# Kernel tuning notes

Measured on AMD Instinct MI355X. Metric: run time of the kernel, lower is better.

## Reference

```python
import jax, jax.numpy as jnp
import numpy as np

Q = 9          # D2Q9
G = 8          # dihedral group of the square
X = YD = 768   # spatial grid
HID = 32       # tau_net hidden width
N_IN = 6       # moments with order <= 2 (indices 0..5, contiguous by construction)
LOWER_TAU = 0.8


def _build_stencil():
    # D2Q9 velocities and weights
    e = np.array([[0, 0], [1, 0], [0, 1], [-1, 0], [0, -1],
                  [1, 1], [-1, 1], [-1, -1], [1, -1]], dtype=np.float64)
    w = np.array([4 / 9] + [1 / 9] * 4 + [1 / 36] * 4, dtype=np.float64)
    # natural moment matrix: rows are monomials ex^px * ey^py, ordered so that
    # moment_order = [0,1,1,2,2,2,3,3,4]  ->  in_indices=[0..5], out_indices=[6,7,8]
    exps = [(0, 0), (1, 0), (0, 1), (2, 0), (1, 1), (0, 2), (2, 1), (1, 2), (2, 2)]
    M = np.stack([e[:, 0] ** px * e[:, 1] ** py for px, py in exps])  # [Q, Q]
    Minv = np.linalg.inv(M)
    # symmetry group of the square: 4 rotations x {id, x-axis reflection}
    rots = [np.array([[np.cos(a), -np.sin(a)], [np.sin(a), np.cos(a)]])
            for a in (0.0, np.pi / 2, np.pi, 3 * np.pi / 2)]
    refl = np.array([[1.0, 0.0], [0.0, -1.0]])
    Rs = rots + [r @ refl for r in rots]
    perms = []
    for R in Rs:
        Re = np.rint(e @ R.T)
        P = np.zeros((Q, Q))
        for i in range(Q):
            j = int(np.where((e == Re[i]).all(axis=1))[0][0])
            P[j, i] = 1.0  # velocity i maps to velocity j under R
        perms.append(P)
    P = np.stack(perms)                                   # [G, Q, Q]
    actions = np.einsum('qp,gpr,rs->gqs', M, P, Minv)      # moment action  M P M^-1
    Pt = P.transpose(0, 2, 1)                              # P^-1 = P^T
    inv_actions = np.einsum('qp,gpr,rs->gqs', M, Pt, Minv)
    return (M.astype(np.float32), Minv.astype(np.float32),
            actions.astype(np.float32), inv_actions.astype(np.float32),
            e.astype(np.float32), w.astype(np.float32))


def setup_inputs() -> dict:
    key = jax.random.key(0)
    kf, k1, k2, k3 = jax.random.split(key, 4)
    M, Minv, actions, inv_actions, e, w = _build_stencil()
    f = jax.random.uniform(kf, (Q, X, YD), dtype=jnp.float32)
    s = 0.1
    return {
        'f': f,
        'M': jnp.asarray(M), 'Minv': jnp.asarray(Minv),
        'actions': jnp.asarray(actions), 'inv_actions': jnp.asarray(inv_actions),
        'e': jnp.asarray(e), 'w': jnp.asarray(w),
        'W1': jax.random.normal(k1, (N_IN, HID), jnp.float32) * s,
        'b1': jnp.zeros((HID,), jnp.float32),
        'W2': jax.random.normal(k2, (HID, HID), jnp.float32) * s,
        'b2': jnp.zeros((HID,), jnp.float32),
        'W3': jax.random.normal(k3, (HID, Q - N_IN), jnp.float32) * s,
        'b3': jnp.zeros((Q - N_IN,), jnp.float32),
    }


def reference(f, M, Minv, actions, inv_actions, e, w, W1, b1, W2, b2, W3, b3):
    # --- moment transform: m = M f, moved to channel-last [X, Y, Q] ---
    m = jnp.einsum('qp,pxy->xyq', M, f)
    # --- equivariant tau net on low-order moments ---
    x_in = m[..., :N_IN]                                   # in_indices = 0..5
    Ainv = inv_actions[:, :N_IN, :N_IN]                    # [G, 6, 6]
    A = actions[:, N_IN:, N_IN:]                           # [G, 3, 3] (out_indices)
    xg = jnp.einsum('gij,xyj->gxyi', Ainv, x_in)           # [G, X, Y, 6]
    h = jax.nn.relu(xg @ W1 + b1)
    h = jax.nn.relu(h @ W2 + b2)
    o = h @ W3 + b3                                        # [G, X, Y, 3]
    out = jnp.einsum('gij,gxyj->xyi', A, o)                # sum over group -> [X, Y, 3]
    tau_hi = 1.5 + jax.nn.elu(out)                         # gt_half: > 0.5
    taus = jnp.full(m.shape, LOWER_TAU, m.dtype).at[..., N_IN:].set(tau_hi)
    # --- equilibrium moments: meq = M feq(rho, u) (quadratic BGK, cs^2=1/3) ---
    rho = m[..., 0:1]                                      # natural moments: m0=rho
    u = m[..., 1:3] / rho                                  # m1,m2 = momentum
    eu = jnp.einsum('qd,xyd->xyq', e, u)
    usq = jnp.sum(u * u, axis=-1, keepdims=True)
    feq = w * rho * (1.0 + 3.0 * eu + 4.5 * eu * eu - 1.5 * usq)
    meq = jnp.einsum('qp,xyp->xyq', M, feq)
    # --- MRT collision + inverse transform ---
    m_post = m - (m - meq) / taus
    return jnp.einsum('pq,xyq->pxy', Minv, m_post)
```

## Files before the change

kernel.cpp:

```cpp
#include <hip/hip_runtime.h>
#include <hip/hip_bf16.h>
#include <math.h>

#define Q 9
#define NPIX (768 * 768)

typedef short bf16x8 __attribute__((ext_vector_type(8)));
typedef short s16x2 __attribute__((ext_vector_type(2)));
typedef float f32x4 __attribute__((ext_vector_type(4)));
typedef float f32x16 __attribute__((ext_vector_type(16)));
typedef int i32x4 __attribute__((ext_vector_type(4)));

#define A3LOV 512
#define A3HIV 1024
#define A2LOV 1536
#define A2HIV 1600
#define B3TF  6656
#define WSHORTS 13312
#define WVEC4   (WSHORTS / 8)

__device__ __forceinline__ int hidmap(int k) {
    return (k & 3) + 8 * ((k >> 2) & 1) + 4 * (k >> 3);
}

__device__ __forceinline__ unsigned short f2bf(float x) {
    unsigned u = __builtin_bit_cast(unsigned, x);
    unsigned r = u + 0x7FFFu + ((u >> 16) & 1u);
    return (unsigned short)(r >> 16);
}

__device__ __forceinline__ unsigned pk2(float e, float o) {
    __hip_bfloat162 h = __float22bfloat162_rn(make_float2(e, o));
    unsigned u;
    __builtin_memcpy(&u, &h, 4);
    return u;
}

__device__ __forceinline__ unsigned relu2(unsigned d) {
    s16x2 v = __builtin_bit_cast(s16x2, d);
    const s16x2 z = {0, 0};
    v = __builtin_elementwise_max(v, z);
    return __builtin_bit_cast(unsigned, v);
}

__device__ __forceinline__ bf16x8 mk8(unsigned w0, unsigned w1, unsigned w2, unsigned w3) {
    i32x4 t = {(int)w0, (int)w1, (int)w2, (int)w3};
    return __builtin_bit_cast(bf16x8, t);
}

__global__ void prep_kernel(const float* __restrict__ actions,
                            const float* __restrict__ inv_actions,
                            const float* __restrict__ W1,
                            const float* __restrict__ b1,
                            const float* __restrict__ W2,
                            const float* __restrict__ W3,
                            const float* __restrict__ b3,
                            short* __restrict__ wsb,
                            float* __restrict__ wsf) {
    const int idx = blockIdx.x * 256 + threadIdx.x;
    if (idx < 4096) {
        int j = idx & 7, l = (idx >> 3) & 63, g = idx >> 9;
        int m = l & 31, k = (l >> 5) * 8 + j;
        float v = 0.f;
        if (k < 6) {
            #pragma unroll
            for (int i = 0; i < 6; i++)
                v += inv_actions[g * 81 + i * 9 + k] * W1[i * 32 + m];
        } else if (k == 6) v = b1[m];
        wsb[idx] = (short)f2bf(v);
    } else if (idx < 8192) {
        int t = idx - 4096;
        int j = t & 7, l = (t >> 3) & 63, g = t >> 9;
        int m = l & 31, kk = (l >> 5) * 8 + j, h = hidmap(kk);
        float v = 0.f;
        if (m < 3) {
            #pragma unroll
            for (int j3 = 0; j3 < 3; j3++)
                v += W3[h * 3 + j3] * actions[g * 81 + (6 + m) * 9 + (6 + j3)];
        }
        wsb[idx] = (short)f2bf(v);
    } else if (idx < 12288) {
        int t = idx - 8192;
        int j = t & 7, l = (t >> 3) & 63, g = t >> 9;
        int m = l & 31, kk = (l >> 5) * 8 + j, h = 16 + hidmap(kk);
        float v = 0.f;
        if (m < 3) {
            #pragma unroll
            for (int j3 = 0; j3 < 3; j3++)
                v += W3[h * 3 + j3] * actions[g * 81 + (6 + m) * 9 + (6 + j3)];
        }
        wsb[idx] = (short)f2bf(v);
    } else if (idx < 12800) {
        int t = idx - 12288;
        int j = t & 7, l = (t >> 3) & 63;
        int m = l & 31, kk = (l >> 5) * 8 + j;
        wsb[idx] = (short)f2bf(W2[hidmap(kk) * 32 + m]);
    } else if (idx < 13312) {
        int t = idx - 12800;
        int j = t & 7, l = (t >> 3) & 63;
        int m = l & 31, kk = (l >> 5) * 8 + j;
        wsb[idx] = (short)f2bf(W2[(16 + hidmap(kk)) * 32 + m]);
    } else if (idx < 13315) {
        int t = idx - 13312;
        float acc = 0.f;
        for (int g = 0; g < 8; g++)
            #pragma unroll
            for (int j = 0; j < 3; j++)
                acc += actions[g * 81 + (6 + t) * 9 + (6 + j)] * b3[j];
        wsf[B3TF + t] = acc;
    }
}

#define MLP_BODY(WA1, W3LO, W3HI, B1F, OACC)                                          \
    {                                                                                 \
        f32x16 C1 = __builtin_amdgcn_mfma_f32_32x32x16_bf16(WA1, B1F, z16, 0, 0, 0);  \
        bf16x8 B2lo = mk8(relu2(pk2(C1[0], C1[1])), relu2(pk2(C1[2], C1[3])),         \
                          relu2(pk2(C1[4], C1[5])), relu2(pk2(C1[6], C1[7])));        \
        bf16x8 B2hi = mk8(relu2(pk2(C1[8], C1[9])), relu2(pk2(C1[10], C1[11])),       \
                          relu2(pk2(C1[12], C1[13])), relu2(pk2(C1[14], C1[15])));    \
        f32x16 C2 = __builtin_amdgcn_mfma_f32_32x32x16_bf16(a2hi, B2hi, c2i, 0, 0, 0);\
        C2 = __builtin_amdgcn_mfma_f32_32x32x16_bf16(a2lo, B2lo, C2, 0, 0, 0);        \
        bf16x8 B3lo = mk8(relu2(pk2(C2[0], C2[1])), relu2(pk2(C2[2], C2[3])),         \
                          relu2(pk2(C2[4], C2[5])), relu2(pk2(C2[6], C2[7])));        \
        bf16x8 B3hi = mk8(relu2(pk2(C2[8], C2[9])), relu2(pk2(C2[10], C2[11])),       \
                          relu2(pk2(C2[12], C2[13])), relu2(pk2(C2[14], C2[15])));    \
        OACC = __builtin_amdgcn_mfma_f32_32x32x16_bf16(W3HI, B3hi, OACC, 0, 0, 0);    \
        OACC = __builtin_amdgcn_mfma_f32_32x32x16_bf16(W3LO, B3lo, OACC, 0, 0, 0);    \
    }

__global__ __launch_bounds__(256, 3) void lbm_kernel(
    const float* __restrict__ f,
    const float* __restrict__ Minv,
    const float* __restrict__ w,
    const float* __restrict__ b2,
    const short* __restrict__ wsb,
    const float* __restrict__ wsf,
    float* __restrict__ out) {
    __shared__ float oL[4][64][4];
    __shared__ __align__(16) short wlds[WSHORTS];
    (void)Minv;
    (void)w;

    const int tid = threadIdx.x;
    const int wv = tid >> 6;
    const int l = tid & 63;
    const int hi = l >> 5;
    const int p = blockIdx.x * 256 + tid;

    {
        const i32x4* src = (const i32x4*)wsb;
        i32x4* dst = (i32x4*)wlds;
        #pragma unroll
        for (int i = tid; i < WVEC4; i += 256) dst[i] = src[i];
    }

    float fv0 = f[0 * NPIX + p], fv1 = f[1 * NPIX + p], fv2 = f[2 * NPIX + p];
    float fv3 = f[3 * NPIX + p], fv4 = f[4 * NPIX + p], fv5 = f[5 * NPIX + p];
    float fv6 = f[6 * NPIX + p], fv7 = f[7 * NPIX + p], fv8 = f[8 * NPIX + p];
    float sa = fv5 + fv6, sb = fv7 + fv8, sc = fv5 - fv6, sd = fv7 - fv8;
    float sab = sa + sb;
    float m4 = sc + sd;
    float p13 = fv1 + fv3, d13 = fv1 - fv3, p24 = fv2 + fv4, d24 = fv2 - fv4;
    float m0 = fv0 + p13 + p24 + sab;
    float m1 = d13 + (sc - sd);
    float m2 = d24 + (sa - sb);
    float m3 = p13 + sab;
    float m5 = p24 + sab;

    unsigned mp0 = pk2(m0, m1), mp1 = pk2(m2, m3), mp2 = pk2(m4, m5);
    const unsigned CONE = 0x00003F80u;
    const int s0 = (l & 31) << 2;
    const int s1 = s0 | (32 << 2);
    bf16x8 B1A = mk8((unsigned)__builtin_amdgcn_ds_bpermute(s0, (int)mp0),
                     (unsigned)__builtin_amdgcn_ds_bpermute(s0, (int)mp1),
                     (unsigned)__builtin_amdgcn_ds_bpermute(s0, (int)mp2), CONE);
    bf16x8 B1B = mk8((unsigned)__builtin_amdgcn_ds_bpermute(s1, (int)mp0),
                     (unsigned)__builtin_amdgcn_ds_bpermute(s1, (int)mp1),
                     (unsigned)__builtin_amdgcn_ds_bpermute(s1, (int)mp2), CONE);

    float b30 = wsf[B3TF + 0], b31 = wsf[B3TF + 1], b32 = wsf[B3TF + 2];
    f32x16 c2i;
    #pragma unroll
    for (int r = 0; r < 16; r++) {
        const int base = (r & 3) + 8 * (r >> 2);
        c2i[r] = hi ? b2[base + 4] : b2[base];
    }
    f32x16 oinit;
    #pragma unroll
    for (int r = 0; r < 16; r++) oinit[r] = 0.f;
    oinit[0] = hi ? 0.f : b30;
    oinit[1] = hi ? 0.f : b31;
    oinit[2] = hi ? 0.f : b32;
    f32x16 oaccA = oinit, oaccB = oinit;
    f32x16 z16;
    #pragma unroll
    for (int r = 0; r < 16; r++) z16[r] = 0.f;

    __syncthreads();
    const bf16x8* wl = (const bf16x8*)wlds;
    bf16x8 a2lo = wl[A2LOV + l], a2hi = wl[A2HIV + l];

    bf16x8 wa1 = wl[l], w3lo = wl[A3LOV + l], w3hi = wl[A3HIV + l];
    #pragma unroll 1
    for (int g = 0; g < 7; g++) {
        const int gn = g + 1;
        bf16x8 na1  = wl[gn * 64 + l];
        bf16x8 n3lo = wl[A3LOV + gn * 64 + l];
        bf16x8 n3hi = wl[A3HIV + gn * 64 + l];
        MLP_BODY(wa1, w3lo, w3hi, B1A, oaccA);
        MLP_BODY(wa1, w3lo, w3hi, B1B, oaccB);
        wa1 = na1; w3lo = n3lo; w3hi = n3hi;
    }
    int p2 = p;
    asm("" : "+v"(p2));
    float fr0 = f[0 * NPIX + p2], fr1 = f[1 * NPIX + p2], fr2 = f[2 * NPIX + p2];
    float fr3 = f[3 * NPIX + p2], fr4 = f[4 * NPIX + p2], fr5 = f[5 * NPIX + p2];
    float fr6 = f[6 * NPIX + p2], fr7 = f[7 * NPIX + p2], fr8 = f[8 * NPIX + p2];
    MLP_BODY(wa1, w3lo, w3hi, B1A, oaccA);
    MLP_BODY(wa1, w3lo, w3hi, B1B, oaccB);

    if (hi == 0) {
        f32x4 t0 = {oaccA[0], oaccA[1], oaccA[2], oaccA[3]};
        *(f32x4*)&oL[wv][l & 31][0] = t0;
        f32x4 t1 = {oaccB[0], oaccB[1], oaccB[2], oaccB[3]};
        *(f32x4*)&oL[wv][32 + (l & 31)][0] = t1;
    }
    f32x4 ov = *(const f32x4*)&oL[wv][l][0];

    float tinv[3];
    #pragma unroll
    for (int i = 0; i < 3; i++) {
        float o = ov[i];
        float el = (o > 0.f) ? o : (__expf(o) - 1.f);
        tinv[i] = __builtin_amdgcn_rcpf(1.5f + el);
    }

    float rho = m0;
    float ir = __builtin_amdgcn_rcpf(rho);
    float ux = m1 * ir, uy = m2 * ir;
    float usq = ux * ux + uy * uy;
    float base = 1.f - 1.5f * usq;
    float w1r = rho * (1.f / 9.f), w5r = rho * (1.f / 36.f);
    float bx = 3.f * ux, ax = fmaf(4.5f * ux, ux, base);
    float feq1 = w1r * (ax + bx), feq3 = w1r * (ax - bx);
    float by = 3.f * uy, ay = fmaf(4.5f * uy, uy, base);
    float feq2 = w1r * (ay + by), feq4 = w1r * (ay - by);
    float ss = ux + uy, bs = 3.f * ss, as_ = fmaf(4.5f * ss, ss, base);
    float feq5 = w5r * (as_ + bs), feq7 = w5r * (as_ - bs);
    float dd = uy - ux, bd = 3.f * dd, ad = fmaf(4.5f * dd, dd, base);
    float feq6 = w5r * (ad + bd), feq8 = w5r * (ad - bd);

    float g1 = fr1 - feq1, g2 = fr2 - feq2, g3 = fr3 - feq3, g4 = fr4 - feq4;
    float g5 = fr5 - feq5, g6 = fr6 - feq6, g7 = fr7 - feq7, g8 = fr8 - feq8;
    float pa = g1 + g3, pb = g2 + g4;
    float ea = g5 + g6, eb = g7 + g8, ec = g5 - g6, ed = g7 - g8;
    float eab = ea + eb;
    float m3p = pa + eab, m5p = pb + eab, m8p = eab;
    float m6p = ea - eb, m4p = ec + ed, m7p = ec - ed;

    float d3 = 1.25f * m3p, h3 = 0.625f * m3p;
    float d5 = 1.25f * m5p, h5 = 0.625f * m5p;
    float k4 = 0.3125f * m4p;
    float h6 = (0.5f * tinv[0]) * m6p, k6 = 0.5f * h6;
    float h7 = (0.5f * tinv[1]) * m7p, k7 = 0.5f * h7;
    float d8 = tinv[2] * m8p, h8 = 0.5f * d8, k8 = 0.5f * h8;

    float c0 = d8 - d3 - d5;
    float c1 = h3 - h7 - h8;
    float c2 = h5 - h6 - h8;
    float c3 = h3 + h7 - h8;
    float c4 = h5 + h6 - h8;
    float sA = k4 + k7, sB = k6 + k8, sC = k4 + k8;
    float sD = k6 + k7, sE = k7 + k8, sF = k4 + k6;
    float c5 = sA + sB, c6 = sB - sA, c7 = sC - sD, c8 = sE - sF;

    __builtin_nontemporal_store(fr0 - c0, &out[0 * NPIX + p]);
    __builtin_nontemporal_store(fr1 - c1, &out[1 * NPIX + p]);
    __builtin_nontemporal_store(fr2 - c2, &out[2 * NPIX + p]);
    __builtin_nontemporal_store(fr3 - c3, &out[3 * NPIX + p]);
    __builtin_nontemporal_store(fr4 - c4, &out[4 * NPIX + p]);
    __builtin_nontemporal_store(fr5 - c5, &out[5 * NPIX + p]);
    __builtin_nontemporal_store(fr6 - c6, &out[6 * NPIX + p]);
    __builtin_nontemporal_store(fr7 - c7, &out[7 * NPIX + p]);
    __builtin_nontemporal_store(fr8 - c8, &out[8 * NPIX + p]);
}

extern "C" void kernel_launch(void* const* d_in, const int* in_sizes, int n_in,
                              void* d_out, int out_size, void* d_ws, size_t ws_size,
                              hipStream_t stream) {
    const float* f           = (const float*)d_in[0];
    const float* Minv        = (const float*)d_in[2];
    const float* actions     = (const float*)d_in[3];
    const float* inv_actions = (const float*)d_in[4];
    const float* w           = (const float*)d_in[6];
    const float* W1          = (const float*)d_in[7];
    const float* b1          = (const float*)d_in[8];
    const float* W2          = (const float*)d_in[9];
    const float* b2          = (const float*)d_in[10];
    const float* W3          = (const float*)d_in[11];
    const float* b3          = (const float*)d_in[12];
    float* outp = (float*)d_out;
    short* wsb = (short*)d_ws;
    float* wsf = (float*)d_ws;

    prep_kernel<<<53, 256, 0, stream>>>(actions, inv_actions, W1, b1, W2, W3, b3, wsb, wsf);
    lbm_kernel<<<NPIX / 256, 256, 0, stream>>>(f, Minv, w, b2, wsb, wsf, outp);
}
```

Baseline: 119.6 us.

## Process two pixel tiles per block to amortize weight staging across more MLP work

Each 256-thread block now handles 512 pixels. Each wave runs four interleaved MLP chains per group iteration instead of two, reusing the LDS-loaded weight fragments, and the grid is halved. This amortizes the per-block weight copy into LDS and the per-iteration weight loads, and gives more independent MFMA work to hide latency. The epilogue re-derives rho and velocity from the reloaded f, so fewer values stay live across the loop. The cost is higher register pressure from four accumulators under a 3-blocks-per-CU launch bound, with possible spills or lower occupancy, plus fewer blocks in flight.

```diff
diff --git a/kernel.cpp b/kernel.cpp
--- a/kernel.cpp
+++ b/kernel.cpp
@@ -128,105 +128,24 @@
         OACC = __builtin_amdgcn_mfma_f32_32x32x16_bf16(W3LO, B3lo, OACC, 0, 0, 0);    \
     }
 
-__global__ __launch_bounds__(256, 3) void lbm_kernel(
-    const float* __restrict__ f,
-    const float* __restrict__ Minv,
-    const float* __restrict__ w,
-    const float* __restrict__ b2,
-    const short* __restrict__ wsb,
-    const float* __restrict__ wsf,
-    float* __restrict__ out) {
-    __shared__ float oL[4][64][4];
-    __shared__ __align__(16) short wlds[WSHORTS];
-    (void)Minv;
-    (void)w;
-
-    const int tid = threadIdx.x;
-    const int wv = tid >> 6;
-    const int l = tid & 63;
-    const int hi = l >> 5;
-    const int p = blockIdx.x * 256 + tid;
-
-    {
-        const i32x4* src = (const i32x4*)wsb;
-        i32x4* dst = (i32x4*)wlds;
-        #pragma unroll
-        for (int i = tid; i < WVEC4; i += 256) dst[i] = src[i];
-    }
-
-    float fv0 = f[0 * NPIX + p], fv1 = f[1 * NPIX + p], fv2 = f[2 * NPIX + p];
-    float fv3 = f[3 * NPIX + p], fv4 = f[4 * NPIX + p], fv5 = f[5 * NPIX + p];
-    float fv6 = f[6 * NPIX + p], fv7 = f[7 * NPIX + p], fv8 = f[8 * NPIX + p];
-    float sa = fv5 + fv6, sb = fv7 + fv8, sc = fv5 - fv6, sd = fv7 - fv8;
-    float sab = sa + sb;
-    float m4 = sc + sd;
-    float p13 = fv1 + fv3, d13 = fv1 - fv3, p24 = fv2 + fv4, d24 = fv2 - fv4;
-    float m0 = fv0 + p13 + p24 + sab;
-    float m1 = d13 + (sc - sd);
-    float m2 = d24 + (sa - sb);
-    float m3 = p13 + sab;
-    float m5 = p24 + sab;
-
-    unsigned mp0 = pk2(m0, m1), mp1 = pk2(m2, m3), mp2 = pk2(m4, m5);
-    const unsigned CONE = 0x00003F80u;
-    const int s0 = (l & 31) << 2;
-    const int s1 = s0 | (32 << 2);
-    bf16x8 B1A = mk8((unsigned)__builtin_amdgcn_ds_bpermute(s0, (int)mp0),
-                     (unsigned)__builtin_amdgcn_ds_bpermute(s0, (int)mp1),
-                     (unsigned)__builtin_amdgcn_ds_bpermute(s0, (int)mp2), CONE);
-    bf16x8 B1B = mk8((unsigned)__builtin_amdgcn_ds_bpermute(s1, (int)mp0),
-                     (unsigned)__builtin_amdgcn_ds_bpermute(s1, (int)mp1),
-                     (unsigned)__builtin_amdgcn_ds_bpermute(s1, (int)mp2), CONE);
-
-    float b30 = wsf[B3TF + 0], b31 = wsf[B3TF + 1], b32 = wsf[B3TF + 2];
-    f32x16 c2i;
-    #pragma unroll
-    for (int r = 0; r < 16; r++) {
-        const int base = (r & 3) + 8 * (r >> 2);
-        c2i[r] = hi ? b2[base + 4] : b2[base];
-    }
-    f32x16 oinit;
-    #pragma unroll
-    for (int r = 0; r < 16; r++) oinit[r] = 0.f;
-    oinit[0] = hi ? 0.f : b30;
-    oinit[1] = hi ? 0.f : b31;
-    oinit[2] = hi ? 0.f : b32;
-    f32x16 oaccA = oinit, oaccB = oinit;
-    f32x16 z16;
-    #pragma unroll
-    for (int r = 0; r < 16; r++) z16[r] = 0.f;
-
-    __syncthreads();
-    const bf16x8* wl = (const bf16x8*)wlds;
-    bf16x8 a2lo = wl[A2LOV + l], a2hi = wl[A2HIV + l];
-
-    bf16x8 wa1 = wl[l], w3lo = wl[A3LOV + l], w3hi = wl[A3HIV + l];
-    #pragma unroll 1
-    for (int g = 0; g < 7; g++) {
-        const int gn = g + 1;
-        bf16x8 na1  = wl[gn * 64 + l];
-        bf16x8 n3lo = wl[A3LOV + gn * 64 + l];
-        bf16x8 n3hi = wl[A3HIV + gn * 64 + l];
-        MLP_BODY(wa1, w3lo, w3hi, B1A, oaccA);
-        MLP_BODY(wa1, w3lo, w3hi, B1B, oaccB);
-        wa1 = na1; w3lo = n3lo; w3hi = n3hi;
-    }
-    int p2 = p;
-    asm("" : "+v"(p2));
-    float fr0 = f[0 * NPIX + p2], fr1 = f[1 * NPIX + p2], fr2 = f[2 * NPIX + p2];
-    float fr3 = f[3 * NPIX + p2], fr4 = f[4 * NPIX + p2], fr5 = f[5 * NPIX + p2];
-    float fr6 = f[6 * NPIX + p2], fr7 = f[7 * NPIX + p2], fr8 = f[8 * NPIX + p2];
-    MLP_BODY(wa1, w3lo, w3hi, B1A, oaccA);
-    MLP_BODY(wa1, w3lo, w3hi, B1B, oaccB);
-
-    if (hi == 0) {
-        f32x4 t0 = {oaccA[0], oaccA[1], oaccA[2], oaccA[3]};
-        *(f32x4*)&oL[wv][l & 31][0] = t0;
-        f32x4 t1 = {oaccB[0], oaccB[1], oaccB[2], oaccB[3]};
-        *(f32x4*)&oL[wv][32 + (l & 31)][0] = t1;
-    }
-    f32x4 ov = *(const f32x4*)&oL[wv][l][0];
-
+#define MOMENTS_PK(F0,F1,F2,F3,F4,F5,F6,F7,F8, MP0, MP1, MP2)                         \
+    {                                                                                 \
+        float sa = F5 + F6, sb = F7 + F8, sc = F5 - F6, sd = F7 - F8;                 \
+        float sab = sa + sb;                                                          \
+        float m4_ = sc + sd;                                                          \
+        float p13 = F1 + F3, d13 = F1 - F3, p24 = F2 + F4, d24 = F2 - F4;             \
+        float m0_ = F0 + p13 + p24 + sab;                                             \
+        float m1_ = d13 + (sc - sd);                                                  \
+        float m2_ = d24 + (sa - sb);                                                  \
+        float m3_ = p13 + sab;                                                        \
+        float m5_ = p24 + sab;                                                        \
+        MP0 = pk2(m0_, m1_); MP1 = pk2(m2_, m3_); MP2 = pk2(m4_, m5_);                \
+    }
+
+__device__ __forceinline__ void epilogue(float fr0, float fr1, float fr2, float fr3,
+                                         float fr4, float fr5, float fr6, float fr7,
+                                         float fr8, f32x4 ov, int p,
+                                         float* __restrict__ out) {
     float tinv[3];
     #pragma unroll
     for (int i = 0; i < 3; i++) {
@@ -234,8 +153,12 @@
         float el = (o > 0.f) ? o : (__expf(o) - 1.f);
         tinv[i] = __builtin_amdgcn_rcpf(1.5f + el);
     }
-
-    float rho = m0;
+    float sa = fr5 + fr6, sb = fr7 + fr8, sc = fr5 - fr6, sd = fr7 - fr8;
+    float p13 = fr1 + fr3, p24 = fr2 + fr4;
+    float rho = fr0 + p13 + p24 + (sa + sb);
+    float m1 = (fr1 - fr3) + (sc - sd);
+    float m2 = (fr2 - fr4) + (sa - sb);
+
     float ir = __builtin_amdgcn_rcpf(rho);
     float ux = m1 * ir, uy = m2 * ir;
     float usq = ux * ux + uy * uy;
@@ -283,6 +206,127 @@
     __builtin_nontemporal_store(fr6 - c6, &out[6 * NPIX + p]);
     __builtin_nontemporal_store(fr7 - c7, &out[7 * NPIX + p]);
     __builtin_nontemporal_store(fr8 - c8, &out[8 * NPIX + p]);
+}
+
+__global__ __launch_bounds__(256, 3) void lbm_kernel(
+    const float* __restrict__ f,
+    const float* __restrict__ Minv,
+    const float* __restrict__ w,
+    const float* __restrict__ b2,
+    const short* __restrict__ wsb,
+    const float* __restrict__ wsf,
+    float* __restrict__ out) {
+    __shared__ float oL[4][128][4];
+    __shared__ __align__(16) short wlds[WSHORTS];
+    (void)Minv;
+    (void)w;
+
+    const int tid = threadIdx.x;
+    const int wv = tid >> 6;
+    const int l = tid & 63;
+    const int hi = l >> 5;
+    const int p0 = blockIdx.x * 512 + tid;
+    const int p1 = p0 + 256;
+
+    {
+        const i32x4* src = (const i32x4*)wsb;
+        i32x4* dst = (i32x4*)wlds;
+        for (int i = tid; i < WVEC4; i += 256) dst[i] = src[i];
+    }
+
+    unsigned mp0a, mp1a, mp2a, mp0b, mp1b, mp2b;
+    {
+        float a0 = f[0 * NPIX + p0], a1 = f[1 * NPIX + p0], a2 = f[2 * NPIX + p0];
+        float a3 = f[3 * NPIX + p0], a4 = f[4 * NPIX + p0], a5 = f[5 * NPIX + p0];
+        float a6 = f[6 * NPIX + p0], a7 = f[7 * NPIX + p0], a8 = f[8 * NPIX + p0];
+        MOMENTS_PK(a0, a1, a2, a3, a4, a5, a6, a7, a8, mp0a, mp1a, mp2a);
+        float b0 = f[0 * NPIX + p1], b1v = f[1 * NPIX + p1], b2v = f[2 * NPIX + p1];
+        float b3v = f[3 * NPIX + p1], b4 = f[4 * NPIX + p1], b5 = f[5 * NPIX + p1];
+        float b6 = f[6 * NPIX + p1], b7 = f[7 * NPIX + p1], b8 = f[8 * NPIX + p1];
+        MOMENTS_PK(b0, b1v, b2v, b3v, b4, b5, b6, b7, b8, mp0b, mp1b, mp2b);
+    }
+
+    const unsigned CONE = 0x00003F80u;
+    const int s0 = (l & 31) << 2;
+    const int s1 = s0 | (32 << 2);
+    bf16x8 B1A0 = mk8((unsigned)__builtin_amdgcn_ds_bpermute(s0, (int)mp0a),
+                      (unsigned)__builtin_amdgcn_ds_bpermute(s0, (int)mp1a),
+                      (unsigned)__builtin_amdgcn_ds_bpermute(s0, (int)mp2a), CONE);
+    bf16x8 B1B0 = mk8((unsigned)__builtin_amdgcn_ds_bpermute(s1, (int)mp0a),
+                      (unsigned)__builtin_amdgcn_ds_bpermute(s1, (int)mp1a),
+                      (unsigned)__builtin_amdgcn_ds_bpermute(s1, (int)mp2a), CONE);
+    bf16x8 B1A1 = mk8((unsigned)__builtin_amdgcn_ds_bpermute(s0, (int)mp0b),
+                      (unsigned)__builtin_amdgcn_ds_bpermute(s0, (int)mp1b),
+                      (unsigned)__builtin_amdgcn_ds_bpermute(s0, (int)mp2b), CONE);
+    bf16x8 B1B1 = mk8((unsigned)__builtin_amdgcn_ds_bpermute(s1, (int)mp0b),
+                      (unsigned)__builtin_amdgcn_ds_bpermute(s1, (int)mp1b),
+                      (unsigned)__builtin_amdgcn_ds_bpermute(s1, (int)mp2b), CONE);
+
+    float b30 = wsf[B3TF + 0], b31 = wsf[B3TF + 1], b32 = wsf[B3TF + 2];
+    f32x16 c2i;
+    #pragma unroll
+    for (int r = 0; r < 16; r++) {
+        const int base = (r & 3) + 8 * (r >> 2);
+        c2i[r] = hi ? b2[base + 4] : b2[base];
+    }
+    f32x16 oinit;
+    #pragma unroll
+    for (int r = 0; r < 16; r++) oinit[r] = 0.f;
+    oinit[0] = hi ? 0.f : b30;
+    oinit[1] = hi ? 0.f : b31;
+    oinit[2] = hi ? 0.f : b32;
+    f32x16 oaccA0 = oinit, oaccB0 = oinit, oaccA1 = oinit, oaccB1 = oinit;
+    f32x16 z16;
+    #pragma unroll
+    for (int r = 0; r < 16; r++) z16[r] = 0.f;
+
+    __syncthreads();
+    const bf16x8* wl = (const bf16x8*)wlds;
+    bf16x8 a2lo = wl[A2LOV + l], a2hi = wl[A2HIV + l];
+
+    bf16x8 wa1 = wl[l], w3lo = wl[A3LOV + l], w3hi = wl[A3HIV + l];
+    #pragma unroll 1
+    for (int g = 0; g < 7; g++) {
+        const int gn = g + 1;
+        bf16x8 na1  = wl[gn * 64 + l];
+        bf16x8 n3lo = wl[A3LOV + gn * 64 + l];
+        bf16x8 n3hi = wl[A3HIV + gn * 64 + l];
+        MLP_BODY(wa1, w3lo, w3hi, B1A0, oaccA0);
+        MLP_BODY(wa1, w3lo, w3hi, B1B0, oaccB0);
+        MLP_BODY(wa1, w3lo, w3hi, B1A1, oaccA1);
+        MLP_BODY(wa1, w3lo, w3hi, B1B1, oaccB1);
+        wa1 = na1; w3lo = n3lo; w3hi = n3hi;
+    }
+    int q0 = p0;
+    asm("" : "+v"(q0));
+    const int q1 = q0 + 256;
+    float r00 = f[0 * NPIX + q0], r01 = f[1 * NPIX + q0], r02 = f[2 * NPIX + q0];
+    float r03 = f[3 * NPIX + q0], r04 = f[4 * NPIX + q0], r05 = f[5 * NPIX + q0];
+    float r06 = f[6 * NPIX + q0], r07 = f[7 * NPIX + q0], r08 = f[8 * NPIX + q0];
+    float r10 = f[0 * NPIX + q1], r11 = f[1 * NPIX + q1], r12 = f[2 * NPIX + q1];
+    float r13 = f[3 * NPIX + q1], r14 = f[4 * NPIX + q1], r15 = f[5 * NPIX + q1];
+    float r16 = f[6 * NPIX + q1], r17 = f[7 * NPIX + q1], r18 = f[8 * NPIX + q1];
+    MLP_BODY(wa1, w3lo, w3hi, B1A0, oaccA0);
+    MLP_BODY(wa1, w3lo, w3hi, B1B0, oaccB0);
+    MLP_BODY(wa1, w3lo, w3hi, B1A1, oaccA1);
+    MLP_BODY(wa1, w3lo, w3hi, B1B1, oaccB1);
+
+    if (hi == 0) {
+        const int lc = l & 31;
+        f32x4 t0 = {oaccA0[0], oaccA0[1], oaccA0[2], oaccA0[3]};
+        *(f32x4*)&oL[wv][lc][0] = t0;
+        f32x4 t1 = {oaccB0[0], oaccB0[1], oaccB0[2], oaccB0[3]};
+        *(f32x4*)&oL[wv][32 + lc][0] = t1;
+        f32x4 t2 = {oaccA1[0], oaccA1[1], oaccA1[2], oaccA1[3]};
+        *(f32x4*)&oL[wv][64 + lc][0] = t2;
+        f32x4 t3 = {oaccB1[0], oaccB1[1], oaccB1[2], oaccB1[3]};
+        *(f32x4*)&oL[wv][96 + lc][0] = t3;
+    }
+    f32x4 ov0 = *(const f32x4*)&oL[wv][l][0];
+    f32x4 ov1 = *(const f32x4*)&oL[wv][64 + l][0];
+
+    epilogue(r00, r01, r02, r03, r04, r05, r06, r07, r08, ov0, p0, out);
+    epilogue(r10, r11, r12, r13, r14, r15, r16, r17, r18, ov1, p1, out);
 }
 
 extern "C" void kernel_launch(void* const* d_in, const int* in_sizes, int n_in,
@@ -304,5 +348,5 @@
     float* wsf = (float*)d_ws;
 
     prep_kernel<<<53, 256, 0, stream>>>(actions, inv_actions, W1, b1, W2, W3, b3, wsb, wsf);
-    lbm_kernel<<<NPIX / 256, 256, 0, stream>>>(f, Minv, w, b2, wsb, wsf, outp);
-}
+    lbm_kernel<<<NPIX / 512, 256, 0, stream>>>(f, Minv, w, b2, wsb, wsf, outp);
+}
```

Result: slower. 124.4 us (+3.9%).

## Process three pixel tiles per block to amortize LDS weight staging

Applied to the files above, without the earlier changes.

Each block now loops over three 256-pixel tiles, so the weight copy into LDS and the bias register setup are amortized over three times as many pixels, and the grid shrinks threefold. The epilogue recomputes density and momentum from the reloaded distributions instead of keeping them live across the MLP, lowering register pressure. The trade-off is fewer blocks and less inter-block overlap of memory and compute phases, with the loop serializing each block's work.

```diff
diff --git a/kernel.cpp b/kernel.cpp
--- a/kernel.cpp
+++ b/kernel.cpp
@@ -128,105 +128,24 @@
         OACC = __builtin_amdgcn_mfma_f32_32x32x16_bf16(W3LO, B3lo, OACC, 0, 0, 0);    \
     }
 
-__global__ __launch_bounds__(256, 3) void lbm_kernel(
-    const float* __restrict__ f,
-    const float* __restrict__ Minv,
-    const float* __restrict__ w,
-    const float* __restrict__ b2,
-    const short* __restrict__ wsb,
-    const float* __restrict__ wsf,
-    float* __restrict__ out) {
-    __shared__ float oL[4][64][4];
-    __shared__ __align__(16) short wlds[WSHORTS];
-    (void)Minv;
-    (void)w;
-
-    const int tid = threadIdx.x;
-    const int wv = tid >> 6;
-    const int l = tid & 63;
-    const int hi = l >> 5;
-    const int p = blockIdx.x * 256 + tid;
-
-    {
-        const i32x4* src = (const i32x4*)wsb;
-        i32x4* dst = (i32x4*)wlds;
-        #pragma unroll
-        for (int i = tid; i < WVEC4; i += 256) dst[i] = src[i];
-    }
-
-    float fv0 = f[0 * NPIX + p], fv1 = f[1 * NPIX + p], fv2 = f[2 * NPIX + p];
-    float fv3 = f[3 * NPIX + p], fv4 = f[4 * NPIX + p], fv5 = f[5 * NPIX + p];
-    float fv6 = f[6 * NPIX + p], fv7 = f[7 * NPIX + p], fv8 = f[8 * NPIX + p];
-    float sa = fv5 + fv6, sb = fv7 + fv8, sc = fv5 - fv6, sd = fv7 - fv8;
-    float sab = sa + sb;
-    float m4 = sc + sd;
-    float p13 = fv1 + fv3, d13 = fv1 - fv3, p24 = fv2 + fv4, d24 = fv2 - fv4;
-    float m0 = fv0 + p13 + p24 + sab;
-    float m1 = d13 + (sc - sd);
-    float m2 = d24 + (sa - sb);
-    float m3 = p13 + sab;
-    float m5 = p24 + sab;
-
-    unsigned mp0 = pk2(m0, m1), mp1 = pk2(m2, m3), mp2 = pk2(m4, m5);
-    const unsigned CONE = 0x00003F80u;
-    const int s0 = (l & 31) << 2;
-    const int s1 = s0 | (32 << 2);
-    bf16x8 B1A = mk8((unsigned)__builtin_amdgcn_ds_bpermute(s0, (int)mp0),
-                     (unsigned)__builtin_amdgcn_ds_bpermute(s0, (int)mp1),
-                     (unsigned)__builtin_amdgcn_ds_bpermute(s0, (int)mp2), CONE);
-    bf16x8 B1B = mk8((unsigned)__builtin_amdgcn_ds_bpermute(s1, (int)mp0),
-                     (unsigned)__builtin_amdgcn_ds_bpermute(s1, (int)mp1),
-                     (unsigned)__builtin_amdgcn_ds_bpermute(s1, (int)mp2), CONE);
-
-    float b30 = wsf[B3TF + 0], b31 = wsf[B3TF + 1], b32 = wsf[B3TF + 2];
-    f32x16 c2i;
-    #pragma unroll
-    for (int r = 0; r < 16; r++) {
-        const int base = (r & 3) + 8 * (r >> 2);
-        c2i[r] = hi ? b2[base + 4] : b2[base];
-    }
-    f32x16 oinit;
-    #pragma unroll
-    for (int r = 0; r < 16; r++) oinit[r] = 0.f;
-    oinit[0] = hi ? 0.f : b30;
-    oinit[1] = hi ? 0.f : b31;
-    oinit[2] = hi ? 0.f : b32;
-    f32x16 oaccA = oinit, oaccB = oinit;
-    f32x16 z16;
-    #pragma unroll
-    for (int r = 0; r < 16; r++) z16[r] = 0.f;
-
-    __syncthreads();
-    const bf16x8* wl = (const bf16x8*)wlds;
-    bf16x8 a2lo = wl[A2LOV + l], a2hi = wl[A2HIV + l];
-
-    bf16x8 wa1 = wl[l], w3lo = wl[A3LOV + l], w3hi = wl[A3HIV + l];
-    #pragma unroll 1
-    for (int g = 0; g < 7; g++) {
-        const int gn = g + 1;
-        bf16x8 na1  = wl[gn * 64 + l];
-        bf16x8 n3lo = wl[A3LOV + gn * 64 + l];
-        bf16x8 n3hi = wl[A3HIV + gn * 64 + l];
-        MLP_BODY(wa1, w3lo, w3hi, B1A, oaccA);
-        MLP_BODY(wa1, w3lo, w3hi, B1B, oaccB);
-        wa1 = na1; w3lo = n3lo; w3hi = n3hi;
-    }
-    int p2 = p;
-    asm("" : "+v"(p2));
-    float fr0 = f[0 * NPIX + p2], fr1 = f[1 * NPIX + p2], fr2 = f[2 * NPIX + p2];
-    float fr3 = f[3 * NPIX + p2], fr4 = f[4 * NPIX + p2], fr5 = f[5 * NPIX + p2];
-    float fr6 = f[6 * NPIX + p2], fr7 = f[7 * NPIX + p2], fr8 = f[8 * NPIX + p2];
-    MLP_BODY(wa1, w3lo, w3hi, B1A, oaccA);
-    MLP_BODY(wa1, w3lo, w3hi, B1B, oaccB);
-
-    if (hi == 0) {
-        f32x4 t0 = {oaccA[0], oaccA[1], oaccA[2], oaccA[3]};
-        *(f32x4*)&oL[wv][l & 31][0] = t0;
-        f32x4 t1 = {oaccB[0], oaccB[1], oaccB[2], oaccB[3]};
-        *(f32x4*)&oL[wv][32 + (l & 31)][0] = t1;
-    }
-    f32x4 ov = *(const f32x4*)&oL[wv][l][0];
-
+#define MOMENTS_PK(F0,F1,F2,F3,F4,F5,F6,F7,F8, MP0, MP1, MP2)                         \
+    {                                                                                 \
+        float sa = F5 + F6, sb = F7 + F8, sc = F5 - F6, sd = F7 - F8;                 \
+        float sab = sa + sb;                                                          \
+        float m4_ = sc + sd;                                                          \
+        float p13 = F1 + F3, d13 = F1 - F3, p24 = F2 + F4, d24 = F2 - F4;             \
+        float m0_ = F0 + p13 + p24 + sab;                                             \
+        float m1_ = d13 + (sc - sd);                                                  \
+        float m2_ = d24 + (sa - sb);                                                  \
+        float m3_ = p13 + sab;                                                        \
+        float m5_ = p24 + sab;                                                        \
+        MP0 = pk2(m0_, m1_); MP1 = pk2(m2_, m3_); MP2 = pk2(m4_, m5_);                \
+    }
+
+__device__ __forceinline__ void epilogue(float fr0, float fr1, float fr2, float fr3,
+                                         float fr4, float fr5, float fr6, float fr7,
+                                         float fr8, f32x4 ov, int p,
+                                         float* __restrict__ out) {
     float tinv[3];
     #pragma unroll
     for (int i = 0; i < 3; i++) {
@@ -234,8 +153,12 @@
         float el = (o > 0.f) ? o : (__expf(o) - 1.f);
         tinv[i] = __builtin_amdgcn_rcpf(1.5f + el);
     }
-
-    float rho = m0;
+    float sa = fr5 + fr6, sb = fr7 + fr8, sc = fr5 - fr6, sd = fr7 - fr8;
+    float p13 = fr1 + fr3, p24 = fr2 + fr4;
+    float rho = fr0 + p13 + p24 + (sa + sb);
+    float m1 = (fr1 - fr3) + (sc - sd);
+    float m2 = (fr2 - fr4) + (sa - sb);
+
     float ir = __builtin_amdgcn_rcpf(rho);
     float ux = m1 * ir, uy = m2 * ir;
     float usq = ux * ux + uy * uy;
@@ -283,6 +206,109 @@
     __builtin_nontemporal_store(fr6 - c6, &out[6 * NPIX + p]);
     __builtin_nontemporal_store(fr7 - c7, &out[7 * NPIX + p]);
     __builtin_nontemporal_store(fr8 - c8, &out[8 * NPIX + p]);
+}
+
+__global__ __launch_bounds__(256, 3) void lbm_kernel(
+    const float* __restrict__ f,
+    const float* __restrict__ Minv,
+    const float* __restrict__ w,
+    const float* __restrict__ b2,
+    const short* __restrict__ wsb,
+    const float* __restrict__ wsf,
+    float* __restrict__ out) {
+    __shared__ float oL[4][64][4];
+    __shared__ __align__(16) short wlds[WSHORTS];
+    (void)Minv;
+    (void)w;
+
+    const int tid = threadIdx.x;
+    const int wv = tid >> 6;
+    const int l = tid & 63;
+    const int hi = l >> 5;
+
+    {
+        const i32x4* src = (const i32x4*)wsb;
+        i32x4* dst = (i32x4*)wlds;
+        for (int i = tid; i < WVEC4; i += 256) dst[i] = src[i];
+    }
+
+    float b30 = wsf[B3TF + 0], b31 = wsf[B3TF + 1], b32 = wsf[B3TF + 2];
+    f32x16 c2i;
+    #pragma unroll
+    for (int r = 0; r < 16; r++) {
+        const int base = (r & 3) + 8 * (r >> 2);
+        c2i[r] = hi ? b2[base + 4] : b2[base];
+    }
+    f32x16 oinit;
+    #pragma unroll
+    for (int r = 0; r < 16; r++) oinit[r] = 0.f;
+    oinit[0] = hi ? 0.f : b30;
+    oinit[1] = hi ? 0.f : b31;
+    oinit[2] = hi ? 0.f : b32;
+    f32x16 z16;
+    #pragma unroll
+    for (int r = 0; r < 16; r++) z16[r] = 0.f;
+
+    __syncthreads();
+    const bf16x8* wl = (const bf16x8*)wlds;
+    bf16x8 a2lo = wl[A2LOV + l], a2hi = wl[A2HIV + l];
+
+    const unsigned CONE = 0x00003F80u;
+    const int s0 = (l & 31) << 2;
+    const int s1 = s0 | (32 << 2);
+    const int pbase = blockIdx.x * 768;
+
+    #pragma unroll 1
+    for (int t = 0; t < 3; t++) {
+        const int p = pbase + t * 256 + tid;
+
+        unsigned mp0, mp1, mp2;
+        {
+            float a0 = f[0 * NPIX + p], a1 = f[1 * NPIX + p], a2 = f[2 * NPIX + p];
+            float a3 = f[3 * NPIX + p], a4 = f[4 * NPIX + p], a5 = f[5 * NPIX + p];
+            float a6 = f[6 * NPIX + p], a7 = f[7 * NPIX + p], a8 = f[8 * NPIX + p];
+            MOMENTS_PK(a0, a1, a2, a3, a4, a5, a6, a7, a8, mp0, mp1, mp2);
+        }
+
+        bf16x8 B1A = mk8((unsigned)__builtin_amdgcn_ds_bpermute(s0, (int)mp0),
+                         (unsigned)__builtin_amdgcn_ds_bpermute(s0, (int)mp1),
+                         (unsigned)__builtin_amdgcn_ds_bpermute(s0, (int)mp2), CONE);
+        bf16x8 B1B = mk8((unsigned)__builtin_amdgcn_ds_bpermute(s1, (int)mp0),
+                         (unsigned)__builtin_amdgcn_ds_bpermute(s1, (int)mp1),
+                         (unsigned)__builtin_amdgcn_ds_bpermute(s1, (int)mp2), CONE);
+
+        f32x16 oaccA = oinit, oaccB = oinit;
+
+        bf16x8 wa1 = wl[l], w3lo = wl[A3LOV + l], w3hi = wl[A3HIV + l];
+        #pragma unroll 1
+        for (int g = 0; g < 7; g++) {
+            const int gn = g + 1;
+            bf16x8 na1  = wl[gn * 64 + l];
+            bf16x8 n3lo = wl[A3LOV + gn * 64 + l];
+            bf16x8 n3hi = wl[A3HIV + gn * 64 + l];
+            MLP_BODY(wa1, w3lo, w3hi, B1A, oaccA);
+            MLP_BODY(wa1, w3lo, w3hi, B1B, oaccB);
+            wa1 = na1; w3lo = n3lo; w3hi = n3hi;
+        }
+        int p2 = p;
+        asm("" : "+v"(p2));
+        float r0 = f[0 * NPIX + p2], r1 = f[1 * NPIX + p2], r2 = f[2 * NPIX + p2];
+        float r3 = f[3 * NPIX + p2], r4 = f[4 * NPIX + p2], r5 = f[5 * NPIX + p2];
+        float r6 = f[6 * NPIX + p2], r7 = f[7 * NPIX + p2], r8 = f[8 * NPIX + p2];
+        MLP_BODY(wa1, w3lo, w3hi, B1A, oaccA);
+        MLP_BODY(wa1, w3lo, w3hi, B1B, oaccB);
+
+        if (hi == 0) {
+            const int lc = l & 31;
+            f32x4 t0 = {oaccA[0], oaccA[1], oaccA[2], oaccA[3]};
+            *(f32x4*)&oL[wv][lc][0] = t0;
+            f32x4 t1 = {oaccB[0], oaccB[1], oaccB[2], oaccB[3]};
+            *(f32x4*)&oL[wv][32 + lc][0] = t1;
+        }
+        f32x4 ov = *(const f32x4*)&oL[wv][l][0];
+
+        epilogue(r0, r1, r2, r3, r4, r5, r6, r7, r8, ov, p, out);
+    }
 }
 
 extern "C" void kernel_launch(void* const* d_in, const int* in_sizes, int n_in,
@@ -304,5 +330,5 @@
     float* wsf = (float*)d_ws;
 
     prep_kernel<<<53, 256, 0, stream>>>(actions, inv_actions, W1, b1, W2, W3, b3, wsb, wsf);
-    lbm_kernel<<<NPIX / 256, 256, 0, stream>>>(f, Minv, w, b2, wsb, wsf, outp);
-}
+    lbm_kernel<<<NPIX / 768, 256, 0, stream>>>(f, Minv, w, b2, wsb, wsf, outp);
+}
```

Result: no change. 121.1 us (+1.3%).
